# Kernel optimization log

Measured on AMD Instinct MI355X. Metric: run time of the kernel, lower is better.

## Reference

```python
import jax, jax.numpy as jnp
import numpy as np

M, D, H, B = 65536, 256, 4, 512  # memory_size, memory_dim, num_heads, batch


def setup_inputs() -> dict:
    key = jax.random.key(0)
    ks = jax.random.split(key, 9)
    s = np.float32(1.0 / np.sqrt(D))
    sg = np.float32(1.0 / np.sqrt(3 * D))
    z = jnp.zeros((D,), jnp.float32)
    return {
        "query": jax.random.normal(ks[0], (B, D), jnp.float32),
        "memory": jax.random.normal(ks[1], (M, D), jnp.float32),
        "Wq": jax.random.normal(ks[2], (D, D), jnp.float32) * s,
        "bq": z,
        "Wk": jax.random.normal(ks[3], (D, D), jnp.float32) * s,
        "bk": z,
        "Wv": jax.random.normal(ks[4], (D, D), jnp.float32) * s,
        "bv": z,
        "Wo": jax.random.normal(ks[5], (D, D), jnp.float32) * s,
        "bo": z,
        "Wg": jax.random.normal(ks[6], (D, 3 * D), jnp.float32) * sg,
        "bg": z,
        "usage": jax.random.uniform(ks[7], (M,), jnp.float32, 0.0, 10.0),
    }


def reference(query, memory, Wq, bq, Wk, bk, Wv, bv, Wo, bo, Wg, bg, usage):
    hd = D // H
    scale = np.float32(1.0 / np.sqrt(hd))
    # multi-head cross-attention read: one query token vs M memory slots
    Q = (query @ Wq.T + bq).reshape(B, H, hd)
    K = (memory @ Wk.T + bk).reshape(M, H, hd)
    V = (memory @ Wv.T + bv).reshape(M, H, hd)
    scores = jnp.einsum('bhd,mhd->bhm', Q, K) * scale  # [B,H,M]
    attn = jax.nn.softmax(scores, axis=-1)
    retrieved = jnp.einsum('bhm,mhd->bhd', attn, V).reshape(B, D) @ Wo.T + bo
    attn_mean = attn.mean(axis=1)  # [B,M], head-averaged weights used by LRU update

    # sequential LRU-gated memory write (torch does this in a python loop over batch)
    def step(carry, xs):
        mem, use = carry
        q_i, r_i, a_i = xs
        lru = jnp.argmin(use)
        mx = jnp.argmax(a_i)
        idx = jnp.where(use[mx] < use.mean(), mx, lru)
        old = mem[idx]
        gate = jax.nn.sigmoid(jnp.concatenate([q_i, old, r_i]) @ Wg.T + bg)
        mem = mem.at[idx].set(gate * q_i + (1.0 - gate) * old)
        use = use.at[idx].add(1.0)
        return (mem, use), None

    (new_memory, new_usage), _ = jax.lax.scan(step, (memory, usage), (query, retrieved, attn_mean))
    return retrieved, new_memory, new_usage
```

## Files before the change

### kernel.cpp

```cpp
#include <hip/hip_runtime.h>
#include <hip/hip_bf16.h>
#include <math.h>

static const size_t OFF_Q     = 0;
static const size_t OFF_GQ    = 131072;
static const size_t OFF_GR    = 262144;
static const size_t OFF_RPRE  = 393216;
static const size_t OFF_QBF   = 524288;
static const size_t OFF_WKBF  = 8978432;
static const size_t OFF_WVBF  = 9011200;
static const size_t OFF_KB    = 9043968;
static const size_t OFF_ZP    = 17432576;
static const size_t OFF_MZ    = 17694720;
static const size_t OFF_AMV   = 17698816;
static const size_t OFF_AMI   = 17764352;
static const size_t OFF_MX    = 17829888;
static const size_t OFF_UMX   = 17830400;
static const size_t OFF_CANDV = 17830912;
static const size_t OFF_CANDI = 17835008;
static const size_t OFF_BSUM  = 17839104;
static const size_t OFF_CNT   = 17839360;
static const size_t OFF_IDXA  = 17839376;
static const size_t OFF_CHAIN = 17839888;

typedef short v8s __attribute__((ext_vector_type(8)));
typedef float f32x4 __attribute__((ext_vector_type(4)));

__device__ __forceinline__ unsigned short f2bf(float f) {
  unsigned int x = __float_as_uint(f);
  unsigned int r = (x + 0x7fffu + ((x >> 16) & 1u)) >> 16;
  return (unsigned short)r;
}

__device__ __forceinline__ void gld16(const void* g, void* l) {
  __builtin_amdgcn_global_load_lds(
      (const __attribute__((address_space(1))) void*)g,
      (__attribute__((address_space(3))) void*)l, 16, 0, 0);
}

__global__ void k_cvt(const float* __restrict__ in, unsigned short* __restrict__ out, int n) {
  int i = (blockIdx.x * 256 + threadIdx.x) * 8;
  if (i + 8 <= n) {
    float4 a = *reinterpret_cast<const float4*>(in + i);
    float4 b = *reinterpret_cast<const float4*>(in + i + 4);
    ushort4 o1 = {f2bf(a.x), f2bf(a.y), f2bf(a.z), f2bf(a.w)};
    ushort4 o2 = {f2bf(b.x), f2bf(b.y), f2bf(b.z), f2bf(b.w)};
    *reinterpret_cast<ushort4*>(out + i) = o1;
    *reinterpret_cast<ushort4*>(out + i + 4) = o2;
  }
}

__global__ void k_qgq(const float* __restrict__ query, const float* __restrict__ Wq,
                      const float* __restrict__ bq, const float* __restrict__ Wg,
                      const float* __restrict__ bg, float* __restrict__ Q,
                      float* __restrict__ Gq, unsigned short* __restrict__ Qbf) {
  __shared__ __align__(16) float qrow[256];
  const int i = blockIdx.x;
  const int d = threadIdx.x;
  qrow[d] = query[(size_t)i * 256 + d];
  __syncthreads();
  const float4* wq = reinterpret_cast<const float4*>(Wq + (size_t)d * 256);
  float acc = 0.f;
#pragma unroll 8
  for (int j4 = 0; j4 < 64; ++j4) {
    float4 w = wq[j4];
    float4 q = *reinterpret_cast<const float4*>(&qrow[j4 * 4]);
    acc += w.x * q.x + w.y * q.y + w.z * q.z + w.w * q.w;
  }
  float qv = acc + bq[d];
  Q[(size_t)i * 256 + d] = qv;
  Qbf[(size_t)i * 256 + d] = f2bf(qv * 0.125f);
  const float4* wg = reinterpret_cast<const float4*>(Wg + (size_t)d * 768);
  float acc2 = 0.f;
#pragma unroll 8
  for (int j4 = 0; j4 < 64; ++j4) {
    float4 w = wg[j4];
    float4 q = *reinterpret_cast<const float4*>(&qrow[j4 * 4]);
    acc2 += w.x * q.x + w.y * q.y + w.z * q.z + w.w * q.w;
  }
  Gq[(size_t)i * 256 + d] = acc2 + bg[d];
}

__global__ __launch_bounds__(256) void k_projmm(const float* __restrict__ mem,
    const unsigned short* __restrict__ Wkbf, const float* __restrict__ bk,
    const unsigned short* __restrict__ Wvbf, const float* __restrict__ bv,
    unsigned short* __restrict__ Kout, unsigned short* __restrict__ Vt) {
  __shared__ __align__(16) char sbuf[36864];
  const int t = threadIdx.x;
  const int w = t >> 6, l = t & 63, l15 = l & 15, lg = l >> 4;
  const int mb = blockIdx.x * 64;
  const int mrow = mb + w * 16 + l15;
  v8s am[8];
#pragma unroll
  for (int kk = 0; kk < 8; ++kk) {
    const float* src = mem + (size_t)mrow * 256 + kk * 32 + lg * 8;
    float4 f0 = *reinterpret_cast<const float4*>(src);
    float4 f1 = *reinterpret_cast<const float4*>(src + 4);
    v8s a;
    a[0] = (short)f2bf(f0.x); a[1] = (short)f2bf(f0.y);
    a[2] = (short)f2bf(f0.z); a[3] = (short)f2bf(f0.w);
    a[4] = (short)f2bf(f1.x); a[5] = (short)f2bf(f1.y);
    a[6] = (short)f2bf(f1.z); a[7] = (short)f2bf(f1.w);
    am[kk] = a;
  }

#define STAGE_W(Wsrc, dt)                                                     \
  {                                                                           \
    _Pragma("unroll")                                                         \
    for (int j = 0; j < 8; ++j) {                                             \
      int off = j * 4096 + w * 1024 + l * 16;                                 \
      int row = off >> 9;                                                     \
      int col = off & 511;                                                    \
      gld16(reinterpret_cast<const char*>(Wsrc) +                             \
                (size_t)((dt) * 64 + row) * 512 + (col ^ ((row & 7) << 4)),   \
            sbuf + j * 4096 + w * 1024);                                      \
    }                                                                         \
  }

  {
    f32x4 acc[16];
#pragma unroll
    for (int df = 0; df < 16; ++df) {
      float bz = bk[df * 16 + l15];
      acc[df] = (f32x4){bz, bz, bz, bz};
    }
    for (int dt = 0; dt < 4; ++dt) {
      STAGE_W(Wkbf, dt);
      asm volatile("s_waitcnt vmcnt(0)" ::: "memory");
      __builtin_amdgcn_s_barrier();
#pragma unroll
      for (int kk = 0; kk < 8; ++kk)
#pragma unroll
        for (int dfl = 0; dfl < 4; ++dfl) {
          const int row = dfl * 16 + l15;
          const v8s b = *reinterpret_cast<const v8s*>(
              sbuf + row * 512 + ((kk * 64 + lg * 16) ^ ((row & 7) << 4)));
          acc[dt * 4 + dfl] =
              __builtin_amdgcn_mfma_f32_16x16x32_bf16(am[kk], b, acc[dt * 4 + dfl], 0, 0, 0);
        }
      asm volatile("" ::: "memory");
      __builtin_amdgcn_s_barrier();
    }
    unsigned short* bounce = reinterpret_cast<unsigned short*>(sbuf);
#pragma unroll
    for (int df = 0; df < 16; ++df)
#pragma unroll
      for (int r = 0; r < 4; ++r)
        bounce[(w * 16 + lg * 4 + r) * 264 + df * 16 + l15] = f2bf(acc[df][r]);
  }
  __syncthreads();
  {
    unsigned short* bounce = reinterpret_cast<unsigned short*>(sbuf);
    int row = t >> 2, quad = t & 3;
    const uint4* src = reinterpret_cast<const uint4*>(&bounce[row * 264 + quad * 64]);
    uint4* dst = reinterpret_cast<uint4*>(Kout + (size_t)(mb + row) * 256 + quad * 64);
#pragma unroll
    for (int x = 0; x < 8; ++x) dst[x] = src[x];
  }
  __syncthreads();
  {
    f32x4 acc[16];
#pragma unroll
    for (int df = 0; df < 16; ++df) {
      float bz = bv[df * 16 + l15];
      acc[df] = (f32x4){bz, bz, bz, bz};
    }
    for (int dt = 0; dt < 4; ++dt) {
      STAGE_W(Wvbf, dt);
      asm volatile("s_waitcnt vmcnt(0)" ::: "memory");
      __builtin_amdgcn_s_barrier();
#pragma unroll
      for (int kk = 0; kk < 8; ++kk)
#pragma unroll
        for (int dfl = 0; dfl < 4; ++dfl) {
          const int row = dfl * 16 + l15;
          const v8s b = *reinterpret_cast<const v8s*>(
              sbuf + row * 512 + ((kk * 64 + lg * 16) ^ ((row & 7) << 4)));
          acc[dt * 4 + dfl] =
              __builtin_amdgcn_mfma_f32_16x16x32_bf16(am[kk], b, acc[dt * 4 + dfl], 0, 0, 0);
        }
      asm volatile("" ::: "memory");
      __builtin_amdgcn_s_barrier();
    }
    unsigned short* bounce = reinterpret_cast<unsigned short*>(sbuf);
#pragma unroll
    for (int df = 0; df < 16; ++df)
#pragma unroll
      for (int r = 0; r < 4; ++r)
        bounce[(df * 16 + l15) * 72 + w * 16 + lg * 4 + r] = f2bf(acc[df][r]);
  }
  __syncthreads();
  {
    const unsigned short* bounce = reinterpret_cast<const unsigned short*>(sbuf);
    const uint4* src = reinterpret_cast<const uint4*>(&bounce[t * 72]);
    uint4* dst = reinterpret_cast<uint4*>(Vt + (size_t)t * 65536 + mb);
#pragma unroll
    for (int x = 0; x < 8; ++x) dst[x] = src[x];
  }
#undef STAGE_W
}

__global__ __launch_bounds__(256, 2) void k_fused(const unsigned short* __restrict__ Qbf,
    const unsigned short* __restrict__ Kb, const unsigned short* __restrict__ Vt,
    float* __restrict__ part2, float* __restrict__ zpart,
    float* __restrict__ amv, int* __restrict__ ami) {
  __shared__ __align__(16) unsigned short KsBuf[2][8192];
  __shared__ __align__(16) unsigned short VsBuf[2][8192];
  __shared__ __align__(16) unsigned short Pl[4][16][40];
  const int mc = blockIdx.x;
  const int qc = blockIdx.y;
  const int t = threadIdx.x;
  const int w = t >> 6, l = t & 63, l15 = l & 15, lg = l >> 4;
  const int qbase = qc * 64 + w * 16;
  const char* Kbc = reinterpret_cast<const char*>(Kb);
  const char* Vtc = reinterpret_cast<const char*>(Vt);
  char* lds_k = reinterpret_cast<char*>(KsBuf);
  char* lds_v = reinterpret_cast<char*>(VsBuf);
  v8s aq[4][2];
#pragma unroll
  for (int h = 0; h < 4; ++h)
#pragma unroll
    for (int kk = 0; kk < 2; ++kk)
      aq[h][kk] = *reinterpret_cast<const v8s*>(
          Qbf + (size_t)(qbase + l15) * 256 + h * 64 + kk * 32 + lg * 8);
  f32x4 racc[4][4] = {};
  float zs[4][4] = {};
  float v1[4], v2[4]; int i1[4], i2[4];
#pragma unroll
  for (int r = 0; r < 4; ++r) { v1[r] = -INFINITY; v2[r] = -INFINITY; i1[r] = 0x7fffffff; i2[r] = 0x7fffffff; }
  const int mbase = mc * 1024;

#define STAGE_K2(bufsel, m0)                                                  \
  {                                                                           \
    _Pragma("unroll")                                                         \
    for (int j = 0; j < 4; ++j) {                                             \
      int off = w * 4096 + j * 1024 + l * 16;                                 \
      int row = off >> 9;                                                     \
      int col = off & 511;                                                    \
      gld16(Kbc + (size_t)((m0) + row) * 512 + (col ^ ((row & 7) << 4)),      \
            lds_k + (bufsel) * 16384 + w * 4096 + j * 1024);                  \
    }                                                                         \
  }
#define STAGE_V2(bufsel, m0)                                                  \
  {                                                                           \
    _Pragma("unroll")                                                         \
    for (int j = 0; j < 4; ++j) {                                             \
      int off = w * 4096 + j * 1024 + l * 16;                                 \
      int row = off >> 6;                                                     \
      int col = off & 63;                                                     \
      gld16(Vtc + (size_t)row * 131072 + (size_t)(m0) * 2 +                   \
                (col ^ (((row >> 1) & 3) << 4)),                              \
            lds_v + (bufsel) * 16384 + w * 4096 + j * 1024);                  \
    }                                                                         \
  }

  STAGE_K2(0, mbase);
  STAGE_V2(0, mbase);
  for (int mt = 0; mt < 32; ++mt) {
    const int m0 = mbase + mt * 32;
    if (mt < 31) {
      STAGE_K2((mt + 1) & 1, m0 + 32);
      STAGE_V2((mt + 1) & 1, m0 + 32);
      asm volatile("s_waitcnt vmcnt(8)" ::: "memory");
    } else {
      asm volatile("s_waitcnt vmcnt(0)" ::: "memory");
    }
    __builtin_amdgcn_s_barrier();
    const char* kbp = lds_k + (mt & 1) * 16384;
    const char* vbp = lds_v + (mt & 1) * 16384;
    float cacc[4][2] = {};
#pragma unroll
    for (int h = 0; h < 4; ++h) {
      f32x4 sacc[2] = {};
#pragma unroll
      for (int nf = 0; nf < 2; ++nf) {
        const int row = nf * 16 + l15;
        const int sw = (row & 7) << 4;
#pragma unroll
        for (int kk = 0; kk < 2; ++kk) {
          const v8s b = *reinterpret_cast<const v8s*>(
              kbp + row * 512 + ((h * 128 + kk * 64 + lg * 16) ^ sw));
          sacc[nf] = __builtin_amdgcn_mfma_f32_16x16x32_bf16(aq[h][kk], b, sacc[nf], 0, 0, 0);
        }
      }
#pragma unroll
      for (int nf = 0; nf < 2; ++nf)
#pragma unroll
        for (int r = 0; r < 4; ++r) {
          float e = __expf(sacc[nf][r]);
          cacc[r][nf] += e;
          zs[r][h] += e;
          Pl[w][lg * 4 + r][nf * 16 + l15] =
              (unsigned short)(__float_as_uint(e) >> 16);
        }
      const v8s pa = *reinterpret_cast<const v8s*>(
          reinterpret_cast<const char*>(&Pl[w][l15][0]) + lg * 16);
#pragma unroll
      for (int df = 0; df < 4; ++df) {
        const int vrow = h * 64 + df * 16 + l15;
        const v8s vb = *reinterpret_cast<const v8s*>(
            vbp + vrow * 64 + ((lg * 16) ^ (((vrow >> 1) & 3) << 4)));
        racc[h][df] = __builtin_amdgcn_mfma_f32_16x16x32_bf16(pa, vb, racc[h][df], 0, 0, 0);
      }
    }
#pragma unroll
    for (int r = 0; r < 4; ++r)
#pragma unroll
      for (int nf = 0; nf < 2; ++nf) {
        float val = cacc[r][nf];
        int idx = m0 + nf * 16 + l15;
        if (val > v1[r] || (val == v1[r] && idx < i1[r])) {
          v2[r] = v1[r]; i2[r] = i1[r]; v1[r] = val; i1[r] = idx;
        } else if (val > v2[r] || (val == v2[r] && idx < i2[r])) {
          v2[r] = val; i2[r] = idx;
        }
      }
    asm volatile("" ::: "memory");
    __builtin_amdgcn_s_barrier();
  }
#undef STAGE_K2
#undef STAGE_V2
#pragma unroll
  for (int h = 0; h < 4; ++h)
#pragma unroll
    for (int df = 0; df < 4; ++df)
#pragma unroll
      for (int r = 0; r < 4; ++r) {
        int q = qbase + lg * 4 + r;
        part2[(size_t)mc * 131072 + (size_t)q * 256 + h * 64 + df * 16 + l15] = racc[h][df][r];
      }
#pragma unroll
  for (int mask = 1; mask <= 8; mask <<= 1)
#pragma unroll
    for (int r = 0; r < 4; ++r)
#pragma unroll
      for (int h = 0; h < 4; ++h)
        zs[r][h] += __shfl_xor(zs[r][h], mask);
  if (l15 == 0) {
#pragma unroll
    for (int r = 0; r < 4; ++r)
#pragma unroll
      for (int h = 0; h < 4; ++h) {
        int q = qbase + lg * 4 + r;
        zpart[((size_t)h * 512 + q) * 64 + mc] = zs[r][h];
      }
  }
#pragma unroll
  for (int mask = 1; mask <= 8; mask <<= 1) {
#pragma unroll
    for (int r = 0; r < 4; ++r) {
      float ov1 = __shfl_xor(v1[r], mask); int oi1 = __shfl_xor(i1[r], mask);
      float ov2 = __shfl_xor(v2[r], mask); int oi2 = __shfl_xor(i2[r], mask);
      bool cGTa = ov1 > v1[r] || (ov1 == v1[r] && oi1 < i1[r]);
      float nv1, nv2; int ni1, ni2;
      if (cGTa) {
        nv1 = ov1; ni1 = oi1;
        bool aGTd = v1[r] > ov2 || (v1[r] == ov2 && i1[r] < oi2);
        nv2 = aGTd ? v1[r] : ov2; ni2 = aGTd ? i1[r] : oi2;
      } else {
        nv1 = v1[r]; ni1 = i1[r];
        bool bGTc = v2[r] > ov1 || (v2[r] == ov1 && i2[r] < oi1);
        nv2 = bGTc ? v2[r] : ov1; ni2 = bGTc ? i2[r] : oi1;
      }
      v1[r] = nv1; i1[r] = ni1; v2[r] = nv2; i2[r] = ni2;
    }
  }
  if (l15 == 0) {
#pragma unroll
    for (int r = 0; r < 4; ++r) {
      int q = qbase + lg * 4 + r;
      amv[((size_t)mc * 512 + q) * 2] = v1[r];
      amv[((size_t)mc * 512 + q) * 2 + 1] = v2[r];
      ami[((size_t)mc * 512 + q) * 2] = i1[r];
      ami[((size_t)mc * 512 + q) * 2 + 1] = i2[r];
    }
  }
}

__global__ void k_zred(const float* __restrict__ zpart, float* __restrict__ MZi) {
  int p = blockIdx.x * 256 + threadIdx.x;
  int h = p >> 9, b = p & 511;
  float Z = 0.f;
  for (int c = 0; c < 64; ++c) Z += zpart[((size_t)h * 512 + b) * 64 + c];
  MZi[(size_t)b * 4 + h] = 1.0f / Z;
}

__global__ void k_rcomb(const float* __restrict__ part2, const float* __restrict__ MZi,
                        float* __restrict__ rpre) {
  int b = blockIdx.x, d = threadIdx.x;
  float s = 0.f;
  for (int c = 0; c < 64; ++c) s += part2[(size_t)c * 131072 + (size_t)b * 256 + d];
  rpre[(size_t)b * 256 + d] = s * MZi[(size_t)b * 4 + (d >> 6)];
}

__global__ __launch_bounds__(256) void k_amax2(const float* __restrict__ Qf,
    const float* __restrict__ Wk, const float* __restrict__ bk,
    const float* __restrict__ memory, const float* __restrict__ MZi,
    const float* __restrict__ amv, const int* __restrict__ ami,
    const float* __restrict__ usage, int* __restrict__ mx, float* __restrict__ umx) {
  __shared__ float u[4][256];
  __shared__ float ch[4];
  __shared__ float qrow[256];
  __shared__ float redv[4];
  __shared__ int redi[4];
  const int row = blockIdx.x, t = threadIdx.x;
  qrow[t] = Qf[(size_t)row * 256 + t];
  __syncthreads();
#pragma unroll
  for (int h = 0; h < 4; ++h) {
    float s = 0.f;
    for (int d = 0; d < 64; ++d) s += qrow[h * 64 + d] * Wk[(size_t)(h * 64 + d) * 256 + t];
    u[h][t] = s;
  }
  if (t < 4) {
    float s = 0.f;
    for (int d = 0; d < 64; ++d) s += qrow[t * 64 + d] * bk[t * 64 + d];
    ch[t] = s;
  }
  __syncthreads();
  const int wv = t >> 6, ln = t & 63;
  const float Zi0 = MZi[(size_t)row * 4 + 0];
  const float Zi1 = MZi[(size_t)row * 4 + 1];
  const float Zi2 = MZi[(size_t)row * 4 + 2];
  const float Zi3 = MZi[(size_t)row * 4 + 3];
  float bestv = -INFINITY; int besti = 0x7fffffff;
  for (int c = wv; c < 128; c += 4) {
    int m = ami[((size_t)(c >> 1) * 512 + row) * 2 + (c & 1)];
    float s0 = 0.f, s1 = 0.f, s2 = 0.f, s3 = 0.f;
#pragma unroll
    for (int k = 0; k < 4; ++k) {
      float mv = memory[(size_t)m * 256 + ln + 64 * k];
      s0 += mv * u[0][ln + 64 * k];
      s1 += mv * u[1][ln + 64 * k];
      s2 += mv * u[2][ln + 64 * k];
      s3 += mv * u[3][ln + 64 * k];
    }
#pragma unroll
    for (int mask = 32; mask >= 1; mask >>= 1) {
      s0 += __shfl_xor(s0, mask); s1 += __shfl_xor(s1, mask);
      s2 += __shfl_xor(s2, mask); s3 += __shfl_xor(s3, mask);
    }
    float a = __expf((s0 + ch[0]) * 0.125f) * Zi0 +
              __expf((s1 + ch[1]) * 0.125f) * Zi1 +
              __expf((s2 + ch[2]) * 0.125f) * Zi2 +
              __expf((s3 + ch[3]) * 0.125f) * Zi3;
    if (a > bestv || (a == bestv && m < besti)) { bestv = a; besti = m; }
  }
  if (ln == 0) { redv[wv] = bestv; redi[wv] = besti; }
  __syncthreads();
  if (t == 0) {
    float bv = -INFINITY; int bi = 0x7fffffff;
#pragma unroll
    for (int q = 0; q < 4; ++q) {
      if (redv[q] > bv || (redv[q] == bv && redi[q] < bi)) { bv = redv[q]; bi = redi[q]; }
    }
    mx[row] = bi;
    umx[row] = usage[bi];
  }
}

__global__ void k_out1(const float* __restrict__ rpre, const float* __restrict__ Wo,
                       const float* __restrict__ bo, const float* __restrict__ Wg,
                       float* __restrict__ retr, float* __restrict__ Gr) {
  __shared__ __align__(16) float rr[256];
  __shared__ __align__(16) float rf[256];
  const int i = blockIdx.x, d = threadIdx.x;
  rr[d] = rpre[(size_t)i * 256 + d];
  __syncthreads();
  const float4* wo = reinterpret_cast<const float4*>(Wo + (size_t)d * 256);
  float acc = 0.f;
#pragma unroll 8
  for (int j4 = 0; j4 < 64; ++j4) {
    float4 w = wo[j4];
    float4 q = *reinterpret_cast<const float4*>(&rr[j4 * 4]);
    acc += w.x * q.x + w.y * q.y + w.z * q.z + w.w * q.w;
  }
  float v = acc + bo[d];
  retr[(size_t)i * 256 + d] = v;
  rf[d] = v;
  __syncthreads();
  const float4* wg = reinterpret_cast<const float4*>(Wg + (size_t)d * 768 + 512);
  float acc2 = 0.f;
#pragma unroll 8
  for (int j4 = 0; j4 < 64; ++j4) {
    float4 w = wg[j4];
    float4 q = *reinterpret_cast<const float4*>(&rf[j4 * 4]);
    acc2 += w.x * q.x + w.y * q.y + w.z * q.z + w.w * q.w;
  }
  Gr[(size_t)i * 256 + d] = acc2;
}

__global__ void k_cand(const float* __restrict__ usage, float* __restrict__ candv,
                       int* __restrict__ candi, int* __restrict__ cnt,
                       float* __restrict__ bsum) {
  __shared__ float sred[256];
  int t = threadIdx.x;
  int g = blockIdx.x * 256 + t;
  float u = usage[g];
  sred[t] = u;
  __syncthreads();
  for (int s = 128; s > 0; s >>= 1) {
    if (t < s) sred[t] += sred[t + s];
    __syncthreads();
  }
  if (t == 0) bsum[blockIdx.x] = sred[0];
  if (u < 0.25f) {
    int pos = atomicAdd(cnt, 1);
    if (pos < 2048) { candv[pos] = u; candi[pos] = g; }
  }
}

__global__ __launch_bounds__(1024) void k_scan(const float* __restrict__ candv_g,
    const int* __restrict__ candi_g, const int* __restrict__ cnt_g,
    const float* __restrict__ bsum, const int* __restrict__ mx,
    const float* __restrict__ umx, const float* __restrict__ usage,
    int* __restrict__ idxA, int* __restrict__ chainA, float* __restrict__ new_usage) {
  __shared__ float bV[256 * 24];
  __shared__ int   bI[256 * 24];
  __shared__ unsigned char cnt8[65536];
  __shared__ int si[2048];
  __shared__ unsigned int bmSeen[2048];
  __shared__ unsigned int bmDup[2048];
  __shared__ unsigned int bmCand[2048];
  __shared__ int idxl[512];
  __shared__ int chl[512];
  __shared__ int bcnt[256];
  __shared__ int bpre[256];
  __shared__ double dred[256];
  __shared__ int totsh;

  const int t = threadIdx.x;
  const int ncg0 = cnt_g[0];
  const int ncg = ncg0 > 2048 ? 2048 : ncg0;

  for (int p = t; p < 2048; p += 1024) {
    si[p] = 0; bmSeen[p] = 0u; bmDup[p] = 0u; bmCand[p] = 0u;
  }
  {
    uint4 z; z.x = 0u; z.y = 0u; z.z = 0u; z.w = 0u;
    uint4* c4 = reinterpret_cast<uint4*>(cnt8);
#pragma unroll
    for (int r = 0; r < 4; ++r) c4[t + r * 1024] = z;
  }
  if (t < 256) { bcnt[t] = 0; dred[t] = (double)bsum[t]; }
  __syncthreads();
  for (int s = 128; s > 0; s >>= 1) {
    if (t < s) dred[t] += dred[t + s];
    __syncthreads();
  }
  if (t < 512) {
    int m = mx[t];
    unsigned bit = 1u << (m & 31);
    unsigned old = atomicOr(&bmSeen[m >> 5], bit);
    if (old & bit) atomicOr(&bmDup[m >> 5], bit);
  }
  for (int p = t; p < ncg; p += 1024) {
    float v = candv_g[p];
    int ix = candi_g[p];
    atomicOr(&bmCand[ix >> 5], 1u << (ix & 31));
    int b = (int)(v * 1024.0f);
    if (b > 255) b = 255;
    int pos = atomicAdd(&bcnt[b], 1);
    if (pos < 24) { bV[b * 24 + pos] = v; bI[b * 24 + pos] = ix; }
  }
  __syncthreads();
  if (t < 256) {
    int n = bcnt[t]; if (n > 24) n = 24;
    bcnt[t] = n;
    bpre[t] = n;
  }
  __syncthreads();
  for (int s2 = 1; s2 < 256; s2 <<= 1) {
    int add = 0;
    if (t < 256 && t >= s2) add = bpre[t - s2];
    __syncthreads();
    if (t < 256) bpre[t] += add;
    __syncthreads();
  }
  if (t < 256) {
    int n = bcnt[t];
    float* bv = bV + t * 24;
    int* bi = bI + t * 24;
    for (int a = 1; a < n; ++a) {
      float v = bv[a]; int ix = bi[a];
      int p = a - 1;
      while (p >= 0) {
        float vp = bv[p];
        int ip = bi[p];
        if (vp < v || (vp == v && ip < ix)) break;
        bv[p + 1] = vp; bi[p + 1] = ip;
        --p;
      }
      bv[p + 1] = v; bi[p + 1] = ix;
    }
    if (t == 255) totsh = bpre[255];
  }
  __syncthreads();
  if (t < 256) {
    int n = bcnt[t];
    int off = bpre[t] - n;
    for (int k = 0; k < n; ++k) {
      int ix = bI[t * 24 + k];
      int tag = (bmSeen[ix >> 5] >> (ix & 31)) & 1;
      si[off + k] = ix | (tag << 30);
    }
  }
  __syncthreads();
  int nc = totsh;
  if (nc < 1) nc = 1;
  if (t < 64) {
    const int lane = t;
    const double sum0 = dred[0];
    int mreg[8]; unsigned ureg[8];
#pragma unroll
    for (int g = 0; g < 8; ++g) {
      const int i = g * 64 + lane;
      int m = mx[i];
      float um = umx[i];
      unsigned bit = 1u << (m & 31);
      bool dirty = ((bmDup[m >> 5] | bmCand[m >> 5]) & bit) != 0;
      float mean = (float)((sum0 + (double)i) * (1.0 / 65536.0));
      bool dec = um < mean;
      mreg[g] = m | (dirty ? 0x10000 : 0) | (dec ? 0x20000 : 0);
      ureg[g] = __float_as_uint(um);
    }
    int ptr = 0;
    int c0 = si[0], c1 = si[1], c2 = si[2], c3 = si[3];

#define SCAN_STEP(G, J)                                                       \
  {                                                                           \
    const int I = (G) * 64 + (J);                                             \
    const int RM = __builtin_amdgcn_readlane(mreg[G], (J));                   \
    const int mxi = RM & 0xFFFF;                                              \
    const int fl = (RM >> 16) & 3;                                            \
    int sel, chain; bool adv;                                                 \
    if (!(fl & 1)) {                                                          \
      if (fl & 2) { sel = mxi; chain = 0; adv = false; }                      \
      else { sel = c0 & 0xFFFF; chain = 0; adv = true; }                      \
    } else {                                                                  \
      const float RU = __uint_as_float(__builtin_amdgcn_readlane(ureg[G], (J))); \
      const int cc = (int)cnt8[mxi];                                          \
      const float mean = (float)((sum0 + (double)I) * (1.0 / 65536.0));       \
      const float uu = RU + (float)cc;                                        \
      const int cand_i = c0 & 0xFFFF;                                         \
      if (uu < mean) { sel = mxi; chain = cc; adv = (mxi == cand_i); }        \
      else { sel = cand_i; chain = 0; adv = true; }                           \
    }                                                                         \
    if (lane == 0) {                                                          \
      cnt8[sel] = (unsigned char)(chain + 1);                                 \
      idxl[I] = sel;                                                          \
      chl[I] = chain;                                                         \
    }                                                                         \
    if (adv) {                                                                \
      for (;;) {                                                              \
        ++ptr;                                                                \
        if (ptr >= nc) {                                                      \
          ptr = nc - 1;                                                       \
          c0 = si[ptr];                                                       \
          c1 = si[ptr + 1 < 2048 ? ptr + 1 : 2047];                           \
          c2 = si[ptr + 2 < 2048 ? ptr + 2 : 2047];                           \
          c3 = si[ptr + 3 < 2048 ? ptr + 3 : 2047];                           \
          break;                                                              \
        }                                                                     \
        c0 = c1; c1 = c2; c2 = c3;                                            \
        c3 = si[ptr + 3 < 2048 ? ptr + 3 : 2047];                             \
        if (!(c0 & (1 << 30))) break;                                         \
        if (cnt8[c0 & 0xFFFF] == 0) break;                                    \
      }                                                                       \
    }                                                                         \
  }

#pragma unroll
    for (int g = 0; g < 8; ++g) {
      for (int j = 0; j < 64; j += 4) {
        SCAN_STEP(g, j + 0);
        SCAN_STEP(g, j + 1);
        SCAN_STEP(g, j + 2);
        SCAN_STEP(g, j + 3);
      }
    }
#undef SCAN_STEP
  }
  __syncthreads();
  if (t < 512) {
    idxA[t] = idxl[t];
    chainA[t] = chl[t];
  }
  for (int p = t; p < 65536; p += 1024) {
    int c = (int)cnt8[p];
    if (c > 0) new_usage[p] = usage[p] + (float)c;
  }
}

__global__ void k_gate0(const int* __restrict__ idxA, const int* __restrict__ chainA,
                        const float* __restrict__ memory, const float* __restrict__ query,
                        const float* __restrict__ Gq, const float* __restrict__ Gr,
                        const float* __restrict__ Wg, float* __restrict__ new_memory) {
  const int i = blockIdx.x;
  if (chainA[i] != 0) return;
  const int sel = idxA[i];
  __shared__ __align__(16) float oldr[256];
  const int d = threadIdx.x;
  oldr[d] = memory[(size_t)sel * 256 + d];
  __syncthreads();
  const float4* wg = reinterpret_cast<const float4*>(Wg + (size_t)d * 768 + 256);
  float acc = Gq[(size_t)i * 256 + d] + Gr[(size_t)i * 256 + d];
#pragma unroll 8
  for (int j4 = 0; j4 < 64; ++j4) {
    float4 w = wg[j4];
    float4 o = *reinterpret_cast<const float4*>(&oldr[j4 * 4]);
    acc += w.x * o.x + w.y * o.y + w.z * o.z + w.w * o.w;
  }
  float g = 1.0f / (1.0f + __expf(-acc));
  new_memory[(size_t)sel * 256 + d] = g * query[(size_t)i * 256 + d] + (1.0f - g) * oldr[d];
}

__global__ void k_chain(const int* __restrict__ idxA, const int* __restrict__ chainA,
                        const float* __restrict__ query, const float* __restrict__ Gq,
                        const float* __restrict__ Gr, const float* __restrict__ Wg,
                        float* __restrict__ new_memory) {
  __shared__ int flags[512];
  __shared__ int idxs[512];
  __shared__ __align__(16) float oldr[256];
  const int j0 = blockIdx.x;
  const int d = threadIdx.x;
  flags[d] = chainA[d]; flags[d + 256] = chainA[d + 256];
  idxs[d] = idxA[d]; idxs[d + 256] = idxA[d + 256];
  __syncthreads();
  if (flags[j0] != 1) return;
  const int slot = idxs[j0];
  for (int i = j0; i < 512; ++i) {
    if (idxs[i] != slot) continue;
    oldr[d] = new_memory[(size_t)slot * 256 + d];
    __syncthreads();
    const float4* wg = reinterpret_cast<const float4*>(Wg + (size_t)d * 768 + 256);
    float acc = Gq[(size_t)i * 256 + d] + Gr[(size_t)i * 256 + d];
#pragma unroll 8
    for (int j4 = 0; j4 < 64; ++j4) {
      float4 w = wg[j4];
      float4 o = *reinterpret_cast<const float4*>(&oldr[j4 * 4]);
      acc += w.x * o.x + w.y * o.y + w.z * o.z + w.w * o.w;
    }
    float g = 1.0f / (1.0f + __expf(-acc));
    new_memory[(size_t)slot * 256 + d] = g * query[(size_t)i * 256 + d] + (1.0f - g) * oldr[d];
    __threadfence();
    __syncthreads();
  }
}

extern "C" void kernel_launch(void* const* d_in, const int* in_sizes, int n_in,
                              void* d_out, int out_size, void* d_ws, size_t ws_size,
                              hipStream_t stream) {
  const float* query  = (const float*)d_in[0];
  const float* memory = (const float*)d_in[1];
  const float* Wq = (const float*)d_in[2];
  const float* bq = (const float*)d_in[3];
  const float* Wk = (const float*)d_in[4];
  const float* bk = (const float*)d_in[5];
  const float* Wv = (const float*)d_in[6];
  const float* bv = (const float*)d_in[7];
  const float* Wo = (const float*)d_in[8];
  const float* bo = (const float*)d_in[9];
  const float* Wg = (const float*)d_in[10];
  const float* bg = (const float*)d_in[11];
  const float* usage = (const float*)d_in[12];

  float* out = (float*)d_out;
  float* retr_out = out;
  float* newmem = out + 131072;
  float* newusage = out + 131072 + 16777216;
  float* part2 = newmem;
  unsigned short* VT = (unsigned short*)(newmem + 8388608);

  float* ws = (float*)d_ws;
  float* Qb    = ws + OFF_Q;
  float* Gqb   = ws + OFF_GQ;
  float* Grb   = ws + OFF_GR;
  float* Rpreb = ws + OFF_RPRE;
  unsigned short* QBF   = (unsigned short*)(ws + OFF_QBF);
  unsigned short* WKBF  = (unsigned short*)(ws + OFF_WKBF);
  unsigned short* WVBF  = (unsigned short*)(ws + OFF_WVBF);
  unsigned short* KB    = (unsigned short*)(ws + OFF_KB);
  float* ZPb   = ws + OFF_ZP;
  float* MZib  = ws + OFF_MZ;
  float* AMVb  = ws + OFF_AMV;
  int*   AMIb  = (int*)(ws + OFF_AMI);
  int*   MXb   = (int*)(ws + OFF_MX);
  float* UMXb  = ws + OFF_UMX;
  float* CANDVb = ws + OFF_CANDV;
  int*   CANDIb = (int*)(ws + OFF_CANDI);
  float* BSUMb  = ws + OFF_BSUM;
  int*   CNTb   = (int*)(ws + OFF_CNT);
  int*   IDXAb  = (int*)(ws + OFF_IDXA);
  int*   CHAINb = (int*)(ws + OFF_CHAIN);

  hipMemsetAsync(CNTb, 0, sizeof(int), stream);

  k_cvt<<<32, 256, 0, stream>>>(Wk, WKBF, 65536);
  k_cvt<<<32, 256, 0, stream>>>(Wv, WVBF, 65536);
  k_qgq<<<512, 256, 0, stream>>>(query, Wq, bq, Wg, bg, Qb, Gqb, QBF);
  k_projmm<<<1024, 256, 0, stream>>>(memory, WKBF, bk, WVBF, bv, KB, VT);
  k_fused<<<dim3(64, 8), 256, 0, stream>>>(QBF, KB, VT, part2, ZPb, AMVb, AMIb);
  k_zred<<<8, 256, 0, stream>>>(ZPb, MZib);
  k_rcomb<<<512, 256, 0, stream>>>(part2, MZib, Rpreb);
  k_amax2<<<512, 256, 0, stream>>>(Qb, Wk, bk, memory, MZib, AMVb, AMIb, usage, MXb, UMXb);
  k_out1<<<512, 256, 0, stream>>>(Rpreb, Wo, bo, Wg, retr_out, Grb);
  k_cand<<<256, 256, 0, stream>>>(usage, CANDVb, CANDIb, CNTb, BSUMb);

  hipMemcpyAsync(newmem, memory, (size_t)16777216 * 4, hipMemcpyDeviceToDevice, stream);
  hipMemcpyAsync(newusage, usage, (size_t)65536 * 4, hipMemcpyDeviceToDevice, stream);

  k_scan<<<1, 1024, 0, stream>>>(CANDVb, CANDIb, CNTb, BSUMb, MXb, UMXb, usage, IDXAb, CHAINb, newusage);
  k_gate0<<<512, 256, 0, stream>>>(IDXAb, CHAINb, memory, query, Gqb, Grb, Wg, newmem);
  k_chain<<<512, 256, 0, stream>>>(IDXAb, CHAINb, query, Gqb, Grb, Wg, newmem);
}
```

Before: 467.6 us.

## Overlap serial LRU scan with rcomb, output projection and memory copy

The single-block sequential scan kernel gets extra blocks in the same launch. Those blocks do the retrieved-vector reduction (rcomb) and copy the second half of the 64 MB memory into the output. A second combined kernel runs the Wo/Wg output projection next to extra blocks that copy the first half of memory, replacing the separate hipMemcpy. The aim is to hide the latency-bound one-block scan and the large copy behind other work. The risk is that the huge shared-memory footprint per block of k_par1 limits occupancy for the helper blocks.

```diff
diff --git a/kernel.cpp b/kernel.cpp
--- a/kernel.cpp
+++ b/kernel.cpp
@@ -385,14 +385,6 @@
   MZi[(size_t)b * 4 + h] = 1.0f / Z;
 }
 
-__global__ void k_rcomb(const float* __restrict__ part2, const float* __restrict__ MZi,
-                        float* __restrict__ rpre) {
-  int b = blockIdx.x, d = threadIdx.x;
-  float s = 0.f;
-  for (int c = 0; c < 64; ++c) s += part2[(size_t)c * 131072 + (size_t)b * 256 + d];
-  rpre[(size_t)b * 256 + d] = s * MZi[(size_t)b * 4 + (d >> 6)];
-}
-
 __global__ __launch_bounds__(256) void k_amax2(const float* __restrict__ Qf,
     const float* __restrict__ Wk, const float* __restrict__ bk,
     const float* __restrict__ memory, const float* __restrict__ MZi,
@@ -459,37 +451,6 @@
   }
 }
 
-__global__ void k_out1(const float* __restrict__ rpre, const float* __restrict__ Wo,
-                       const float* __restrict__ bo, const float* __restrict__ Wg,
-                       float* __restrict__ retr, float* __restrict__ Gr) {
-  __shared__ __align__(16) float rr[256];
-  __shared__ __align__(16) float rf[256];
-  const int i = blockIdx.x, d = threadIdx.x;
-  rr[d] = rpre[(size_t)i * 256 + d];
-  __syncthreads();
-  const float4* wo = reinterpret_cast<const float4*>(Wo + (size_t)d * 256);
-  float acc = 0.f;
-#pragma unroll 8
-  for (int j4 = 0; j4 < 64; ++j4) {
-    float4 w = wo[j4];
-    float4 q = *reinterpret_cast<const float4*>(&rr[j4 * 4]);
-    acc += w.x * q.x + w.y * q.y + w.z * q.z + w.w * q.w;
-  }
-  float v = acc + bo[d];
-  retr[(size_t)i * 256 + d] = v;
-  rf[d] = v;
-  __syncthreads();
-  const float4* wg = reinterpret_cast<const float4*>(Wg + (size_t)d * 768 + 512);
-  float acc2 = 0.f;
-#pragma unroll 8
-  for (int j4 = 0; j4 < 64; ++j4) {
-    float4 w = wg[j4];
-    float4 q = *reinterpret_cast<const float4*>(&rf[j4 * 4]);
-    acc2 += w.x * q.x + w.y * q.y + w.z * q.z + w.w * q.w;
-  }
-  Gr[(size_t)i * 256 + d] = acc2;
-}
-
 __global__ void k_cand(const float* __restrict__ usage, float* __restrict__ candv,
                        int* __restrict__ candi, int* __restrict__ cnt,
                        float* __restrict__ bsum) {
@@ -510,11 +471,14 @@
   }
 }
 
-__global__ __launch_bounds__(1024) void k_scan(const float* __restrict__ candv_g,
+__global__ __launch_bounds__(1024) void k_par1(const float* __restrict__ candv_g,
     const int* __restrict__ candi_g, const int* __restrict__ cnt_g,
     const float* __restrict__ bsum, const int* __restrict__ mx,
     const float* __restrict__ umx, const float* __restrict__ usage,
-    int* __restrict__ idxA, int* __restrict__ chainA, float* __restrict__ new_usage) {
+    int* __restrict__ idxA, int* __restrict__ chainA, float* __restrict__ new_usage,
+    const float* __restrict__ part2, const float* __restrict__ MZi,
+    float* __restrict__ rpre, const float* __restrict__ memory,
+    float* __restrict__ newmem) {
   __shared__ float bV[256 * 24];
   __shared__ int   bI[256 * 24];
   __shared__ unsigned char cnt8[65536];
@@ -529,7 +493,28 @@
   __shared__ double dred[256];
   __shared__ int totsh;
 
+  const int bid = blockIdx.x;
   const int t = threadIdx.x;
+
+  if (bid >= 129) {
+    const size_t base = 8388608 + (size_t)(bid - 129) * 8192;
+#pragma unroll
+    for (int j = 0; j < 2; ++j) {
+      size_t idx = base + (size_t)j * 4096 + (size_t)t * 4;
+      *reinterpret_cast<float4*>(newmem + idx) =
+          *reinterpret_cast<const float4*>(memory + idx);
+    }
+    return;
+  }
+  if (bid >= 1) {
+    const int b = (bid - 1) * 4 + (t >> 8);
+    const int d = t & 255;
+    float s = 0.f;
+    for (int c = 0; c < 64; ++c) s += part2[(size_t)c * 131072 + (size_t)b * 256 + d];
+    rpre[(size_t)b * 256 + d] = s * MZi[(size_t)b * 4 + (d >> 6)];
+    return;
+  }
+
   const int ncg0 = cnt_g[0];
   const int ncg = ncg0 > 2048 ? 2048 : ncg0;
 
@@ -692,6 +677,50 @@
   }
 }
 
+__global__ __launch_bounds__(256) void k_par2(const float* __restrict__ rpre,
+    const float* __restrict__ Wo, const float* __restrict__ bo,
+    const float* __restrict__ Wg, float* __restrict__ retr, float* __restrict__ Gr,
+    const float* __restrict__ memory, float* __restrict__ newmem) {
+  __shared__ __align__(16) float rr[256];
+  __shared__ __align__(16) float rf[256];
+  const int bid = blockIdx.x;
+  const int t = threadIdx.x;
+  if (bid >= 512) {
+    const size_t base = (size_t)(bid - 512) * 8192;
+#pragma unroll
+    for (int j = 0; j < 8; ++j) {
+      size_t idx = base + (size_t)j * 1024 + (size_t)t * 4;
+      *reinterpret_cast<float4*>(newmem + idx) =
+          *reinterpret_cast<const float4*>(memory + idx);
+    }
+    return;
+  }
+  const int i = bid, d = t;
+  rr[d] = rpre[(size_t)i * 256 + d];
+  __syncthreads();
+  const float4* wo = reinterpret_cast<const float4*>(Wo + (size_t)d * 256);
+  float acc = 0.f;
+#pragma unroll 8
+  for (int j4 = 0; j4 < 64; ++j4) {
+    float4 w = wo[j4];
+    float4 q = *reinterpret_cast<const float4*>(&rr[j4 * 4]);
+    acc += w.x * q.x + w.y * q.y + w.z * q.z + w.w * q.w;
+  }
+  float v = acc + bo[d];
+  retr[(size_t)i * 256 + d] = v;
+  rf[d] = v;
+  __syncthreads();
+  const float4* wg = reinterpret_cast<const float4*>(Wg + (size_t)d * 768 + 512);
+  float acc2 = 0.f;
+#pragma unroll 8
+  for (int j4 = 0; j4 < 64; ++j4) {
+    float4 w = wg[j4];
+    float4 q = *reinterpret_cast<const float4*>(&rf[j4 * 4]);
+    acc2 += w.x * q.x + w.y * q.y + w.z * q.z + w.w * q.w;
+  }
+  Gr[(size_t)i * 256 + d] = acc2;
+}
+
 __global__ void k_gate0(const int* __restrict__ idxA, const int* __restrict__ chainA,
                         const float* __restrict__ memory, const float* __restrict__ query,
                         const float* __restrict__ Gq, const float* __restrict__ Gr,
@@ -802,15 +831,16 @@
   k_projmm<<<1024, 256, 0, stream>>>(memory, WKBF, bk, WVBF, bv, KB, VT);
   k_fused<<<dim3(64, 8), 256, 0, stream>>>(QBF, KB, VT, part2, ZPb, AMVb, AMIb);
   k_zred<<<8, 256, 0, stream>>>(ZPb, MZib);
-  k_rcomb<<<512, 256, 0, stream>>>(part2, MZib, Rpreb);
   k_amax2<<<512, 256, 0, stream>>>(Qb, Wk, bk, memory, MZib, AMVb, AMIb, usage, MXb, UMXb);
-  k_out1<<<512, 256, 0, stream>>>(Rpreb, Wo, bo, Wg, retr_out, Grb);
   k_cand<<<256, 256, 0, stream>>>(usage, CANDVb, CANDIb, CNTb, BSUMb);
 
-  hipMemcpyAsync(newmem, memory, (size_t)16777216 * 4, hipMemcpyDeviceToDevice, stream);
   hipMemcpyAsync(newusage, usage, (size_t)65536 * 4, hipMemcpyDeviceToDevice, stream);
 
-  k_scan<<<1, 1024, 0, stream>>>(CANDVb, CANDIb, CNTb, BSUMb, MXb, UMXb, usage, IDXAb, CHAINb, newusage);
+  k_par1<<<1153, 1024, 0, stream>>>(CANDVb, CANDIb, CNTb, BSUMb, MXb, UMXb, usage,
+                                    IDXAb, CHAINb, newusage, part2, MZib, Rpreb,
+                                    memory, newmem);
+  k_par2<<<1536, 256, 0, stream>>>(Rpreb, Wo, bo, Wg, retr_out, Grb, memory, newmem);
+
   k_gate0<<<512, 256, 0, stream>>>(IDXAb, CHAINb, memory, query, Gqb, Grb, Wg, newmem);
   k_chain<<<512, 256, 0, stream>>>(IDXAb, CHAINb, query, Gqb, Grb, Wg, newmem);
 }
```

New measurement: 448.3 us. -4.1%, faster.
